# Kernel tuning notes

Measured on AMD Instinct MI355X. Metric: run time of the kernel, lower is better.

The kernel has to match this reference:

```python
import jax, jax.numpy as jnp
import numpy as np

OUTDIM, INPUTDIM, DEGREE = 64, 512, 8


def setup_inputs() -> dict:
    key = jax.random.key(0)
    k1, k2 = jax.random.split(key)
    x = jax.random.normal(k1, (16, 4096, INPUTDIM), dtype=jnp.float32)
    # torch.randn(outdim, inputdim, degree) / (sqrt(inputdim)*sqrt(degree))
    coeffs = jax.random.normal(k2, (OUTDIM, INPUTDIM, DEGREE), dtype=jnp.float32)
    coeffs = coeffs / (np.sqrt(INPUTDIM) * np.sqrt(DEGREE))
    bias = jnp.zeros((1, OUTDIM), dtype=jnp.float32)
    return {"x": x, "coeffs": coeffs, "bias": bias}


def _legendre_basis(xn, degree):
    # Iterative (memoized) Legendre recurrence; xn in [-1, 1], shape [N, I].
    Ps = [jnp.ones_like(xn)]
    if degree > 1:
        Ps.append(xn)
    for n in range(2, degree):
        Ps.append(((2.0 * n - 1.0) * xn * Ps[-1] - (n - 1.0) * Ps[-2]) / n)
    return jnp.stack(Ps, axis=-1)  # [N, I, D]


def reference(x, coeffs, bias):
    outdim, inputdim, degree = coeffs.shape
    outshape = x.shape[:-1] + (outdim,)
    x2 = x.reshape(-1, inputdim)                      # [N, I]
    xmin, xmax = x2.min(), x2.max()                   # global min-max normalize
    xn = 2.0 * (x2 - xmin) / (xmax - xmin) - 1.0
    P = _legendre_basis(xn, degree)                   # [N, I, D]
    y = jnp.einsum("nid,oid->no", P, coeffs)          # contract input & degree
    y = y + bias                                      # [N, O]
    return y.reshape(outshape)
```

## Files before the change

kernel.cpp:

```cpp
#include <hip/hip_runtime.h>
#include <math.h>


typedef __bf16 bf16x8 __attribute__((ext_vector_type(8)));
typedef float f32x4 __attribute__((ext_vector_type(4)));

__device__ __forceinline__ void gload_lds16(const float* g, void* lds) {
  __builtin_amdgcn_global_load_lds(
      static_cast<const unsigned int*>(static_cast<const void*>(g)),
      static_cast<unsigned int*>(lds), 16, 0, 0);
}

__global__ __launch_bounds__(256) void k_pre(
    const float4* __restrict__ x4, int n4,
    float* __restrict__ pmn, float* __restrict__ pmx,
    const float* __restrict__ coeffs, bf16x8* __restrict__ Bws, int doprep)
{
  if (doprep && blockIdx.x < 128) {
    int t = blockIdx.x * 256 + threadIdx.x;
    int lane = t & 63;
    int tile = t >> 6;
    int ct = tile & 3;
    int kt = tile >> 2;
    int ii = kt * 4 + (lane >> 4);
    int o  = ct * 16 + (lane & 15);
    const float4* cp = (const float4*)(coeffs + ((size_t)o * 512 + ii) * 8);
    float4 c0 = cp[0], c1 = cp[1];
    bf16x8 v;
    v[0] = (__bf16)(c0.x);
    v[1] = (__bf16)(c0.y);
    v[2] = (__bf16)(c0.z * 1.5f);
    v[3] = (__bf16)(c0.w * 2.5f);
    v[4] = (__bf16)(c1.x * 4.375f);
    v[5] = (__bf16)(c1.y * 7.875f);
    v[6] = (__bf16)(c1.z * 14.4375f);
    v[7] = (__bf16)(c1.w * 26.8125f);
    Bws[(size_t)(kt * 4 + ct) * 64 + lane] = v;
  }
  float mn = 3.4e38f, mx = -3.4e38f;
  int stride = gridDim.x * 256;
  for (int i = blockIdx.x * 256 + threadIdx.x; i < n4; i += stride) {
    float4 v = x4[i];
    mn = fminf(mn, fminf(fminf(v.x, v.y), fminf(v.z, v.w)));
    mx = fmaxf(mx, fmaxf(fmaxf(v.x, v.y), fmaxf(v.z, v.w)));
  }
  #pragma unroll
  for (int off = 32; off > 0; off >>= 1) {
    mn = fminf(mn, __shfl_down(mn, off));
    mx = fmaxf(mx, __shfl_down(mx, off));
  }
  __shared__ float smn[4], smx[4];
  int w = threadIdx.x >> 6;
  if ((threadIdx.x & 63) == 0) { smn[w] = mn; smx[w] = mx; }
  __syncthreads();
  if (threadIdx.x == 0) {
    pmn[blockIdx.x] = fminf(fminf(smn[0], smn[1]), fminf(smn[2], smn[3]));
    pmx[blockIdx.x] = fmaxf(fmaxf(smx[0], smx[1]), fmaxf(smx[2], smx[3]));
  }
}

#define NPART 2048
__global__ __launch_bounds__(256, 3) void k_main(
    const float* __restrict__ x, const bf16x8* __restrict__ Bws,
    const float* __restrict__ bias, const float* __restrict__ pmn,
    const float* __restrict__ pmx, float* __restrict__ y)
{
  __shared__ __attribute__((aligned(16))) char smem[49152];

  const int t    = threadIdx.x;
  const int lane = t & 63;
  const int w    = t >> 6;
  const int m    = lane & 15;
  const int quad = lane >> 4;
  const size_t blockRow = (size_t)blockIdx.x * 64;

  const float* gp[4];
  #pragma unroll
  for (int p = 0; p < 4; ++p) {
    int r15 = 4 * p + quad;
    int row = 16 * w + r15;
    int cfl = m ^ r15;
    gp[p] = x + (size_t)(blockRow + row) * 512 + cfl * 4;
  }
  #pragma unroll
  for (int p = 0; p < 4; ++p)
    gload_lds16(gp[p], smem + (w * 4 + p) * 1024);

  float mn = 3.4e38f, mx = -3.4e38f;
  #pragma unroll
  for (int j = 0; j < NPART / 64; ++j) {
    mn = fminf(mn, pmn[lane + j * 64]);
    mx = fmaxf(mx, pmx[lane + j * 64]);
  }
  #pragma unroll
  for (int o2 = 32; o2 > 0; o2 >>= 1) {
    mn = fminf(mn, __shfl_xor(mn, o2));
    mx = fmaxf(mx, __shfl_xor(mx, o2));
  }
  const float s   = 2.0f / (mx - mn);
  const float off = fmaf(-mn, s, -1.0f);

  bf16x8 Bq[4][4];
  #pragma unroll
  for (int ct = 0; ct < 4; ++ct) {
    Bq[0][ct] = Bws[(size_t)((4 * w + 0) * 4 + ct) * 64 + lane];
    Bq[1][ct] = Bws[(size_t)((4 * w + 1) * 4 + ct) * 64 + lane];
  }

  f32x4 acc[4][4];
  #pragma unroll
  for (int f = 0; f < 4; ++f)
    #pragma unroll
    for (int ct = 0; ct < 4; ++ct) acc[f][ct] = (f32x4){0.f, 0.f, 0.f, 0.f};

  int xbase[4], xo[4];
  #pragma unroll
  for (int f = 0; f < 4; ++f) xbase[f] = (f * 16 + m) * 64 + quad;
  #pragma unroll
  for (int k = 0; k < 4; ++k) xo[k] = ((4 * w + k) ^ m) << 2;

  const float C2 = 0.33333334f, C3 = 0.26666668f, C4 = 0.25714287f;
  const float C5 = 0.25396827f, C6 = 0.25252524f, C7 = 0.25174826f;

  __syncthreads();

  for (int c = 0; c < 8; ++c) {
    const float* xr = (const float*)(smem + (c & 1) * 16384);

    if (c < 7) {
      char* lb = smem + ((c + 1) & 1) * 16384;
      #pragma unroll
      for (int p = 0; p < 4; ++p)
        gload_lds16(gp[p] + (c + 1) * 64, lb + (w * 4 + p) * 1024);
    }

    float xvv[2][4];
    #pragma unroll
    for (int f = 0; f < 4; ++f) xvv[0][f] = xr[xbase[f] + xo[0]];

    #pragma unroll
    for (int ktl = 0; ktl < 4; ++ktl) {
      const int l = c * 4 + ktl;

      {
        const int lp  = (l + 2) & 31;
        const int ktg = ((lp >> 2) << 4) + 4 * w + (lp & 3);
        #pragma unroll
        for (int ct = 0; ct < 4; ++ct)
          Bq[(ktl + 2) & 3][ct] = Bws[(size_t)(ktg * 4 + ct) * 64 + lane];
      }
      if (ktl < 3) {
        #pragma unroll
        for (int f = 0; f < 4; ++f)
          xvv[(ktl + 1) & 1][f] = xr[xbase[f] + xo[ktl + 1]];
      }

      #pragma unroll
      for (int f = 0; f < 4; ++f) {
        float xn = fmaf(xvv[ktl & 1][f], s, off);
        float s2 = fmaf(xn, xn, -C2);
        float s3 = (s2 - C3) * xn;
        float s4 = fmaf(xn, s3, -(C4 * s2));
        float s5 = fmaf(xn, s4, -(C5 * s3));
        float s6 = fmaf(xn, s5, -(C6 * s4));
        float s7 = fmaf(xn, s6, -(C7 * s5));
        bf16x8 av;
        av[0] = (__bf16)1.0f; av[1] = (__bf16)xn; av[2] = (__bf16)s2; av[3] = (__bf16)s3;
        av[4] = (__bf16)s4;   av[5] = (__bf16)s5; av[6] = (__bf16)s6; av[7] = (__bf16)s7;
        #pragma unroll
        for (int ct = 0; ct < 4; ++ct)
          acc[f][ct] = __builtin_amdgcn_mfma_f32_16x16x32_bf16(av, Bq[ktl & 3][ct], acc[f][ct], 0, 0, 0);
      }
    }
    __syncthreads();
  }

  f32x4* red = (f32x4*)smem;
  if (w > 0) {
    #pragma unroll
    for (int f = 0; f < 4; ++f)
      #pragma unroll
      for (int ct = 0; ct < 4; ++ct)
        red[(size_t)(w - 1) * 1024 + (f * 4 + ct) * 64 + lane] = acc[f][ct];
  }
  __syncthreads();
  if (w == 0) {
    #pragma unroll
    for (int f = 0; f < 4; ++f)
      #pragma unroll
      for (int ct = 0; ct < 4; ++ct) {
        f32x4 v = acc[f][ct];
        v += red[(f * 4 + ct) * 64 + lane];
        v += red[1024 + (f * 4 + ct) * 64 + lane];
        v += red[2048 + (f * 4 + ct) * 64 + lane];
        acc[f][ct] = v;
      }
    float bv0 = bias[m], bv1 = bias[16 + m], bv2 = bias[32 + m], bv3 = bias[48 + m];
    #pragma unroll
    for (int f = 0; f < 4; ++f) {
      float* yp = y + (blockRow + f * 16 + quad * 4) * 64 + m;
      #pragma unroll
      for (int r = 0; r < 4; ++r) {
        float* ypr = yp + r * 64;
        ypr[0]  = acc[f][0][r] + bv0;
        ypr[16] = acc[f][1][r] + bv1;
        ypr[32] = acc[f][2][r] + bv2;
        ypr[48] = acc[f][3][r] + bv3;
      }
    }
  }
}

__global__ __launch_bounds__(256) void k_so(
    const float* __restrict__ pmn, const float* __restrict__ pmx, int nb,
    float* __restrict__ so)
{
  float mn = 3.4e38f, mx = -3.4e38f;
  for (int i = threadIdx.x; i < nb; i += 256) {
    mn = fminf(mn, pmn[i]);
    mx = fmaxf(mx, pmx[i]);
  }
  #pragma unroll
  for (int off = 32; off > 0; off >>= 1) {
    mn = fminf(mn, __shfl_down(mn, off));
    mx = fmaxf(mx, __shfl_down(mx, off));
  }
  __shared__ float smn[4], smx[4];
  int w = threadIdx.x >> 6;
  if ((threadIdx.x & 63) == 0) { smn[w] = mn; smx[w] = mx; }
  __syncthreads();
  if (threadIdx.x == 0) {
    mn = fminf(fminf(smn[0], smn[1]), fminf(smn[2], smn[3]));
    mx = fmaxf(fmaxf(smx[0], smx[1]), fmaxf(smx[2], smx[3]));
    float r = mx - mn;
    so[0] = 2.0f / r;
    so[1] = -2.0f * mn / r - 1.0f;
  }
}

__global__ __launch_bounds__(256) void k_main_simple(
    const float* __restrict__ x, const float* __restrict__ coeffs,
    const float* __restrict__ bias, const float* __restrict__ so, float* __restrict__ y)
{
  const float s = so[0], off = so[1];
  const int lane = threadIdx.x & 63;
  const int w    = threadIdx.x >> 6;
  const int m    = lane & 15;
  const int quad = lane >> 4;
  const int rowA = blockIdx.x * 64 + w * 16 + m;
  const float* xp = x + (size_t)rowA * 512 + quad;

  f32x4 acc0 = {0.f,0.f,0.f,0.f}, acc1 = acc0, acc2 = acc0, acc3 = acc0;
  const float c3a = 5.f/3.f, c3b = 2.f/3.f, c6a = 11.f/6.f, c6b = 5.f/6.f, c7a = 13.f/7.f, c7b = 6.f/7.f;

  for (int kt = 0; kt < 128; ++kt) {
    float xv = xp[kt * 4];
    int i = kt * 4 + quad;
    bf16x8 b[4];
    #pragma unroll
    for (int ct = 0; ct < 4; ++ct) {
      const float* cp = coeffs + ((size_t)(ct * 16 + m) * 512 + i) * 8;
      #pragma unroll
      for (int j = 0; j < 8; ++j) b[ct][j] = (__bf16)cp[j];
    }
    float xn = fmaf(xv, s, off);
    float p2 = fmaf(1.5f * xn, xn, -0.5f);
    float p3 = fmaf(c3a * xn, p2, -(c3b * xn));
    float p4 = fmaf(1.75f * xn, p3, -(0.75f * p2));
    float p5 = fmaf(1.8f * xn, p4, -(0.8f * p3));
    float p6 = fmaf(c6a * xn, p5, -(c6b * p4));
    float p7 = fmaf(c7a * xn, p6, -(c7b * p5));
    bf16x8 a;
    a[0] = (__bf16)1.0f; a[1] = (__bf16)xn; a[2] = (__bf16)p2; a[3] = (__bf16)p3;
    a[4] = (__bf16)p4;   a[5] = (__bf16)p5; a[6] = (__bf16)p6; a[7] = (__bf16)p7;
    acc0 = __builtin_amdgcn_mfma_f32_16x16x32_bf16(a, b[0], acc0, 0, 0, 0);
    acc1 = __builtin_amdgcn_mfma_f32_16x16x32_bf16(a, b[1], acc1, 0, 0, 0);
    acc2 = __builtin_amdgcn_mfma_f32_16x16x32_bf16(a, b[2], acc2, 0, 0, 0);
    acc3 = __builtin_amdgcn_mfma_f32_16x16x32_bf16(a, b[3], acc3, 0, 0, 0);
  }
  float b0v = bias[m], b1v = bias[16+m], b2v = bias[32+m], b3v = bias[48+m];
  float* yp = y + ((size_t)(blockIdx.x * 64 + w * 16 + quad * 4)) * 64 + m;
  #pragma unroll
  for (int r = 0; r < 4; ++r) {
    yp[r*64+ 0] = acc0[r] + b0v;
    yp[r*64+16] = acc1[r] + b1v;
    yp[r*64+32] = acc2[r] + b2v;
    yp[r*64+48] = acc3[r] + b3v;
  }
}

extern "C" void kernel_launch(void* const* d_in, const int* in_sizes, int n_in,
                              void* d_out, int out_size, void* d_ws, size_t ws_size,
                              hipStream_t stream)
{
  const float* x      = (const float*)d_in[0];
  const float* coeffs = (const float*)d_in[1];
  const float* bias   = (const float*)d_in[2];
  float* y = (float*)d_out;

  long nx = (long)in_sizes[0];
  int  N  = (int)(nx / 512);
  int  n4 = (int)(nx / 4);

  float*  so  = (float*)d_ws;
  float*  pmn = (float*)d_ws + 16;
  float*  pmx = pmn + 4096;
  bf16x8* Bws = (bf16x8*)((char*)d_ws + 65536);

  bool pre = ws_size >= (size_t)(65536 + 4096 * 64 * 2 + 4096);
  k_pre<<<NPART, 256, 0, stream>>>((const float4*)x, n4, pmn, pmx, coeffs, Bws, pre ? 1 : 0);
  if (pre) {
    k_main<<<N / 64, 256, 0, stream>>>(x, Bws, bias, pmn, pmx, y);
  } else {
    k_so<<<1, 256, 0, stream>>>(pmn, pmx, NPART, so);
    k_main_simple<<<N / 64, 256, 0, stream>>>(x, coeffs, bias, so, y);
  }
}
```

Measured before the change: 242.0 us.

## Split cross-wave reduction across all waves and shrink B prefetch buffer

The cross-wave reduction now has each wave own one 16-row fragment group. Every wave writes its other three groups to LDS, then sums and stores its own group, so wave 0 no longer does all the reduction and output stores alone. Separately, the B-operand register prefetch is cut from a 4-deep ring (two slices ahead) to double buffering (one slice ahead). This lowers register pressure but exposes more global-load latency before each MFMA group.

```diff
diff --git a/kernel.cpp b/kernel.cpp
--- a/kernel.cpp
+++ b/kernel.cpp
@@ -100,12 +100,10 @@
   const float s   = 2.0f / (mx - mn);
   const float off = fmaf(-mn, s, -1.0f);
 
-  bf16x8 Bq[4][4];
-  #pragma unroll
-  for (int ct = 0; ct < 4; ++ct) {
+  bf16x8 Bq[2][4];
+  #pragma unroll
+  for (int ct = 0; ct < 4; ++ct)
     Bq[0][ct] = Bws[(size_t)((4 * w + 0) * 4 + ct) * 64 + lane];
-    Bq[1][ct] = Bws[(size_t)((4 * w + 1) * 4 + ct) * 64 + lane];
-  }
 
   f32x4 acc[4][4];
   #pragma unroll
@@ -143,11 +141,11 @@
       const int l = c * 4 + ktl;
 
       {
-        const int lp  = (l + 2) & 31;
+        const int lp  = (l + 1) & 31;
         const int ktg = ((lp >> 2) << 4) + 4 * w + (lp & 3);
         #pragma unroll
         for (int ct = 0; ct < 4; ++ct)
-          Bq[(ktl + 2) & 3][ct] = Bws[(size_t)(ktg * 4 + ct) * 64 + lane];
+          Bq[(ktl + 1) & 1][ct] = Bws[(size_t)(ktg * 4 + ct) * 64 + lane];
       }
       if (ktl < 3) {
         #pragma unroll
@@ -169,44 +167,42 @@
         av[4] = (__bf16)s4;   av[5] = (__bf16)s5; av[6] = (__bf16)s6; av[7] = (__bf16)s7;
         #pragma unroll
         for (int ct = 0; ct < 4; ++ct)
-          acc[f][ct] = __builtin_amdgcn_mfma_f32_16x16x32_bf16(av, Bq[ktl & 3][ct], acc[f][ct], 0, 0, 0);
+          acc[f][ct] = __builtin_amdgcn_mfma_f32_16x16x32_bf16(av, Bq[ktl & 1][ct], acc[f][ct], 0, 0, 0);
       }
     }
     __syncthreads();
   }
 
   f32x4* red = (f32x4*)smem;
-  if (w > 0) {
-    #pragma unroll
-    for (int f = 0; f < 4; ++f)
+  #pragma unroll
+  for (int g = 0; g < 4; ++g) {
+    if (g != w) {
+      int slot = w - (w > g ? 1 : 0);
       #pragma unroll
       for (int ct = 0; ct < 4; ++ct)
-        red[(size_t)(w - 1) * 1024 + (f * 4 + ct) * 64 + lane] = acc[f][ct];
+        red[(size_t)g * 768 + slot * 256 + ct * 64 + lane] = acc[g][ct];
+    }
   }
   __syncthreads();
-  if (w == 0) {
-    #pragma unroll
-    for (int f = 0; f < 4; ++f)
-      #pragma unroll
-      for (int ct = 0; ct < 4; ++ct) {
-        f32x4 v = acc[f][ct];
-        v += red[(f * 4 + ct) * 64 + lane];
-        v += red[1024 + (f * 4 + ct) * 64 + lane];
-        v += red[2048 + (f * 4 + ct) * 64 + lane];
-        acc[f][ct] = v;
-      }
+  {
     float bv0 = bias[m], bv1 = bias[16 + m], bv2 = bias[32 + m], bv3 = bias[48 + m];
-    #pragma unroll
-    for (int f = 0; f < 4; ++f) {
-      float* yp = y + (blockRow + f * 16 + quad * 4) * 64 + m;
-      #pragma unroll
-      for (int r = 0; r < 4; ++r) {
-        float* ypr = yp + r * 64;
-        ypr[0]  = acc[f][0][r] + bv0;
-        ypr[16] = acc[f][1][r] + bv1;
-        ypr[32] = acc[f][2][r] + bv2;
-        ypr[48] = acc[f][3][r] + bv3;
-      }
+    f32x4 vv[4];
+    #pragma unroll
+    for (int ct = 0; ct < 4; ++ct) {
+      f32x4 v = acc[w][ct];
+      v += red[(size_t)w * 768 + 0 * 256 + ct * 64 + lane];
+      v += red[(size_t)w * 768 + 1 * 256 + ct * 64 + lane];
+      v += red[(size_t)w * 768 + 2 * 256 + ct * 64 + lane];
+      vv[ct] = v;
+    }
+    float* yp = y + (blockRow + w * 16 + quad * 4) * 64 + m;
+    #pragma unroll
+    for (int r = 0; r < 4; ++r) {
+      float* ypr = yp + r * 64;
+      ypr[0]  = vv[0][r] + bv0;
+      ypr[16] = vv[1][r] + bv1;
+      ypr[32] = vv[2][r] + bv2;
+      ypr[48] = vv[3][r] + bv3;
     }
   }
 }
```

Result: slower. 350.6 us (+44.9%).
